# Optimization experiments

Hardware: AMD Instinct MI355X
Metric: run time of the kernel (lower is better)

The kernel has to match this reference:

```python
import jax, jax.numpy as jnp
import numpy as np


def setup_inputs() -> dict:
    key = jax.random.key(0)
    k1, k2, k3, k4 = jax.random.split(key, 4)
    N, F, E, M = 50000, 128, 1600000, 1024
    return {
        "molec_feature_vectures": jax.random.normal(k1, (N, F), dtype=jnp.float32),
        "W": jax.random.normal(k2, (F, F), dtype=jnp.float32),
        "mo_neighbour_indices": jax.random.randint(k3, (2, E), 0, N, dtype=jnp.int64),
        "mo_mol_id": jax.random.randint(k4, (E,), 0, M, dtype=jnp.int64),
        "n_output": M,
    }


def reference(molec_feature_vectures, W, mo_neighbour_indices, mo_mol_id, n_output):
    # Gather endpoint features for each neighbor pair: [E, F]
    fi = molec_feature_vectures[mo_neighbour_indices[0]]
    fj = molec_feature_vectures[mo_neighbour_indices[1]]
    # Symmetric bilinear form (mode='pes'): s_n = fi_n . (W + W^T) . fj_n
    Ws = W + W.T  # [F, F]
    # Fuse as (fi @ Ws) * fj summed over F to avoid a 3-operand einsum blowup
    scalars = jnp.einsum('ni,ij,nj->n', fi, Ws, fj)  # [E]
    # Segment-sum per molecule
    res = jax.ops.segment_sum(scalars, mo_mol_id, num_segments=n_output)  # [M]
    return res
```

## Files before the change

### kernel.cpp

```cpp
#include <hip/hip_runtime.h>
#include <hip/hip_bf16.h>

#define FDIM 128
#define BROWS 32
#define NBLK 256
#define NSLICE 32

typedef __attribute__((ext_vector_type(8))) short short8v;
typedef __attribute__((ext_vector_type(4))) float f32x4;
typedef __attribute__((ext_vector_type(2))) _Float16 half2v;

static __device__ __forceinline__ unsigned short f2bf(float x) {
    unsigned u = __float_as_uint(x);
    unsigned r = 0x7fffu + ((u >> 16) & 1u);
    return (unsigned short)((u + r) >> 16);
}
static __device__ __forceinline__ float bf2f(unsigned short h) {
    return __uint_as_float((unsigned)h << 16);
}
static __device__ __forceinline__ void split2(float v, short& h, short& l) {
    unsigned short hh = f2bf(v);
    h = (short)hh;
    l = (short)f2bf(v - bf2f(hh));
}

static __device__ __forceinline__ half2v u2h(unsigned u) {
    union { unsigned u; half2v h; } c; c.u = u; return c.h;
}
static __device__ __forceinline__ unsigned pack2h(float a, float b) {
    union { unsigned u; half2v h; } c;
    c.h[0] = (_Float16)a; c.h[1] = (_Float16)b; return c.u;
}
static __device__ __forceinline__ unsigned short f2h(float x) {
    union { unsigned short s; _Float16 h; } c; c.h = (_Float16)x; return c.s;
}
static __device__ __forceinline__ float fdot2(half2v a, half2v b, float c) {
#if defined(__has_builtin) && __has_builtin(__builtin_amdgcn_fdot2)
    return __builtin_amdgcn_fdot2(a, b, c, false);
#else
    return fmaf((float)a[1], (float)b[1], fmaf((float)a[0], (float)b[0], c));
#endif
}

__global__ __launch_bounds__(1024) void k_ws_hist(
    const float* __restrict__ W,
    unsigned short* __restrict__ WsH, unsigned short* __restrict__ WsL,
    const int* __restrict__ idx, int E, int nb, unsigned* __restrict__ M) {
    if (blockIdx.x >= NBLK) {
        int i2 = (blockIdx.x - NBLK) * 1024 + threadIdx.x;
        int i = i2 >> 7, j = i2 & 127;
        float w = W[i2] + W[j * 128 + i];
        short h, l;
        split2(w, h, l);
        WsH[i2] = (unsigned short)h;
        WsL[i2] = (unsigned short)l;
        return;
    }
    extern __shared__ unsigned cnt[];
    for (int i = threadIdx.x; i < nb; i += 1024) cnt[i] = 0;
    __syncthreads();
    int chunk = (E + NBLK - 1) / NBLK;
    int s = blockIdx.x * chunk;
    int e_end = min(E, s + chunk);
    for (int e = s + threadIdx.x; e < e_end; e += 1024) {
        int i1 = idx[E + e];
        atomicAdd(&cnt[i1 >> 5], 1u);
    }
    __syncthreads();
    for (int i = threadIdx.x; i < nb; i += 1024)
        M[(size_t)blockIdx.x * nb + i] = cnt[i];
}

__global__ __launch_bounds__(512, 4) void gemm_mfma(
    const float* __restrict__ Fm,
    const unsigned short* __restrict__ WsH, const unsigned short* __restrict__ WsL,
    unsigned short* __restrict__ Gh, int N) {
    __shared__ __align__(16) unsigned short sH[128 * 136];
    __shared__ __align__(16) unsigned short sL[128 * 136];

    for (int k = threadIdx.x; k < 128 * 16; k += 512) {
        int i = k >> 4, g = k & 15;
        *(uint4*)((char*)sH + i * 272 + g * 16) =
            *(const uint4*)((const char*)WsH + i * 256 + g * 16);
        *(uint4*)((char*)sL + i * 272 + g * 16) =
            *(const uint4*)((const char*)WsL + i * 256 + g * 16);
    }
    __syncthreads();

    const int wid  = threadIdx.x >> 6;
    const int lane = threadIdx.x & 63;
    const int ar   = lane & 15;
    const int kg   = lane >> 4;
    const int row0 = blockIdx.x * 128 + wid * 16;
    const int gr   = row0 + ar;
    const bool rv  = gr < N;
    const float* fp = Fm + (size_t)gr * FDIM;

    f32x4 acc[8];
#pragma unroll
    for (int t = 0; t < 8; ++t) acc[t] = (f32x4){0.f, 0.f, 0.f, 0.f};

#pragma unroll
    for (int ks = 0; ks < 4; ++ks) {
        const int k0 = ks * 32 + kg * 8;
        float4 fa = make_float4(0.f, 0.f, 0.f, 0.f);
        float4 fb = make_float4(0.f, 0.f, 0.f, 0.f);
        if (rv) {
            fa = *(const float4*)(fp + k0);
            fb = *(const float4*)(fp + k0 + 4);
        }
        short8v ah, al;
        {
            short h, l;
            split2(fa.x, h, l); ah[0] = h; al[0] = l;
            split2(fa.y, h, l); ah[1] = h; al[1] = l;
            split2(fa.z, h, l); ah[2] = h; al[2] = l;
            split2(fa.w, h, l); ah[3] = h; al[3] = l;
            split2(fb.x, h, l); ah[4] = h; al[4] = l;
            split2(fb.y, h, l); ah[5] = h; al[5] = l;
            split2(fb.z, h, l); ah[6] = h; al[6] = l;
            split2(fb.w, h, l); ah[7] = h; al[7] = l;
        }
#pragma unroll
        for (int ct = 0; ct < 8; ++ct) {
            const short8v bh = *(const short8v*)(sH + (ct * 16 + ar) * 136 + k0);
            const short8v bl = *(const short8v*)(sL + (ct * 16 + ar) * 136 + k0);
            acc[ct] = __builtin_amdgcn_mfma_f32_16x16x32_bf16(ah, bh, acc[ct], 0, 0, 0);
            acc[ct] = __builtin_amdgcn_mfma_f32_16x16x32_bf16(ah, bl, acc[ct], 0, 0, 0);
            acc[ct] = __builtin_amdgcn_mfma_f32_16x16x32_bf16(al, bh, acc[ct], 0, 0, 0);
        }
    }

#pragma unroll
    for (int r = 0; r < 4; ++r) {
        const int orow = row0 + kg * 4 + r;
        if (orow < N) {
#pragma unroll
            for (int ct = 0; ct < 8; ++ct)
                Gh[(size_t)orow * FDIM + ct * 16 + ar] = f2h(acc[ct][r]);
        }
    }
}

__global__ __launch_bounds__(256) void k_mscan2(unsigned* __restrict__ M, int nb,
                                                unsigned* __restrict__ tot) {
    int b = blockIdx.x * 4 + (threadIdx.x >> 6);
    int lane = threadIdx.x & 63;
    if (b >= nb) return;
    unsigned m0 = M[(size_t)(4 * lane + 0) * nb + b];
    unsigned m1 = M[(size_t)(4 * lane + 1) * nb + b];
    unsigned m2 = M[(size_t)(4 * lane + 2) * nb + b];
    unsigned m3 = M[(size_t)(4 * lane + 3) * nb + b];
    unsigned s = m0 + m1 + m2 + m3;
    unsigned incl = s;
#pragma unroll
    for (int d = 1; d < 64; d <<= 1) {
        unsigned u = __shfl_up(incl, d, 64);
        if (lane >= d) incl += u;
    }
    unsigned run = incl - s;
    M[(size_t)(4 * lane + 0) * nb + b] = run; run += m0;
    M[(size_t)(4 * lane + 1) * nb + b] = run; run += m1;
    M[(size_t)(4 * lane + 2) * nb + b] = run; run += m2;
    M[(size_t)(4 * lane + 3) * nb + b] = run;
    if (lane == 63) tot[b] = incl;
}

__global__ __launch_bounds__(1024) void k_scatter(const int* __restrict__ idx,
                                                  const int* __restrict__ mol, int E,
                                                  int nb, const unsigned* __restrict__ M,
                                                  const unsigned* __restrict__ tot,
                                                  unsigned* __restrict__ bucketStart,
                                                  unsigned* __restrict__ sortedE) {
    extern __shared__ unsigned cur[];
    __shared__ unsigned wTot[16];

    const int t = threadIdx.x;
    const int lane = t & 63, wid = t >> 6;
    const int b0 = 2 * t;
    unsigned a0 = (b0 < nb) ? tot[b0] : 0u;
    unsigned a1 = (b0 + 1 < nb) ? tot[b0 + 1] : 0u;
    unsigned tsum = a0 + a1;
    unsigned incl = tsum;
#pragma unroll
    for (int d = 1; d < 64; d <<= 1) {
        unsigned u = __shfl_up(incl, d, 64);
        if (lane >= d) incl += u;
    }
    if (lane == 63) wTot[wid] = incl;
    __syncthreads();
    unsigned wOff = 0;
    for (int i = 0; i < wid; ++i) wOff += wTot[i];
    const unsigned base = wOff + incl - tsum;
    if (b0 < nb)     cur[b0]     = M[(size_t)blockIdx.x * nb + b0] + base;
    if (b0 + 1 < nb) cur[b0 + 1] = M[(size_t)blockIdx.x * nb + b0 + 1] + base + a0;
    if (blockIdx.x == 0) {
        if (b0 < nb)     bucketStart[b0]     = base;
        if (b0 + 1 < nb) bucketStart[b0 + 1] = base + a0;
        if (t == 1023)   bucketStart[nb]     = wOff + incl;
    }
    __syncthreads();

    int chunk = (E + NBLK - 1) / NBLK;
    int s = blockIdx.x * chunk;
    int e_end = min(E, s + chunk);
    for (int e = s + threadIdx.x; e < e_end; e += 1024) {
        int i0 = idx[e];
        int i1 = idx[E + e];
        int m  = mol[e];
        int b  = i1 >> 5;
        int loc = i1 & 31;
        unsigned pos = atomicAdd(&cur[b], 1u);
        sortedE[pos] = (unsigned)i0 | ((unsigned)m << 16) | ((unsigned)loc << 26);
    }
}

__global__ __launch_bounds__(512, 6) void edge_kernel(
    const unsigned short* __restrict__ Gh, const float* __restrict__ Fm,
    const unsigned* __restrict__ sortedE, const unsigned* __restrict__ bucketStart,
    float* __restrict__ part, int N, int Mout) {
    __shared__ __align__(16) unsigned short sFrow[BROWS * FDIM];
    __shared__ float smol[1024];

    const int b = blockIdx.x;
    const int row0 = b * BROWS;
    const int nrow = min(BROWS, N - row0);

    for (int k = threadIdx.x; k < nrow * 16; k += 512) {
        int r = k >> 4, g = k & 15;
        const float4* src = (const float4*)(Fm + (size_t)(row0 + r) * FDIM + g * 8);
        float4 v0 = src[0], v1 = src[1];
        uint4 u;
        u.x = pack2h(v0.x, v0.y);
        u.y = pack2h(v0.z, v0.w);
        u.z = pack2h(v1.x, v1.y);
        u.w = pack2h(v1.z, v1.w);
        *(uint4*)(sFrow + r * FDIM + g * 8) = u;
    }
    for (int i = threadIdx.x; i < 1024; i += 512) smol[i] = 0.f;
    __syncthreads();

    const int s = (int)bucketStart[b];
    const int e_end = (int)bucketStart[b + 1];
    const int lane = threadIdx.x & 63;
    const int sub  = lane >> 4;
    const int t16  = lane & 15;
    const int off16 = t16 * 8;
    const int wid  = threadIdx.x >> 6;

#define DOT8(p, g, f) \
    p = fdot2(u2h((g).x), u2h((f).x), p); \
    p = fdot2(u2h((g).y), u2h((f).y), p); \
    p = fdot2(u2h((g).z), u2h((f).z), p); \
    p = fdot2(u2h((g).w), u2h((f).w), p);

    int base = s + wid * 16;

    unsigned pc0 = 0u, pc1 = 0u, pc2 = 0u, pc3 = 0u;
    unsigned pn0 = 0u, pn1 = 0u, pn2 = 0u, pn3 = 0u;
    if (base + sub < e_end)      pc0 = sortedE[base + sub];
    if (base + 4 + sub < e_end)  pc1 = sortedE[base + 4 + sub];
    if (base + 8 + sub < e_end)  pc2 = sortedE[base + 8 + sub];
    if (base + 12 + sub < e_end) pc3 = sortedE[base + 12 + sub];
    {
        const int nx = base + 128;
        if (nx + sub < e_end)      pn0 = sortedE[nx + sub];
        if (nx + 4 + sub < e_end)  pn1 = sortedE[nx + 4 + sub];
        if (nx + 8 + sub < e_end)  pn2 = sortedE[nx + 8 + sub];
        if (nx + 12 + sub < e_end) pn3 = sortedE[nx + 12 + sub];
    }
    uint4 gc0 = *(const uint4*)(Gh + (size_t)(pc0 & 0xffffu) * FDIM + off16);
    uint4 gc1 = *(const uint4*)(Gh + (size_t)(pc1 & 0xffffu) * FDIM + off16);
    uint4 gc2 = *(const uint4*)(Gh + (size_t)(pc2 & 0xffffu) * FDIM + off16);
    uint4 gc3 = *(const uint4*)(Gh + (size_t)(pc3 & 0xffffu) * FDIM + off16);

    while (base < e_end) {
        const uint4 gn0 = *(const uint4*)(Gh + (size_t)(pn0 & 0xffffu) * FDIM + off16);
        const uint4 gn1 = *(const uint4*)(Gh + (size_t)(pn1 & 0xffffu) * FDIM + off16);
        const uint4 gn2 = *(const uint4*)(Gh + (size_t)(pn2 & 0xffffu) * FDIM + off16);
        const uint4 gn3 = *(const uint4*)(Gh + (size_t)(pn3 & 0xffffu) * FDIM + off16);
        const int pf = base + 256;
        unsigned p20 = 0u, p21 = 0u, p22 = 0u, p23 = 0u;
        if (pf + sub < e_end)      p20 = sortedE[pf + sub];
        if (pf + 4 + sub < e_end)  p21 = sortedE[pf + 4 + sub];
        if (pf + 8 + sub < e_end)  p22 = sortedE[pf + 8 + sub];
        if (pf + 12 + sub < e_end) p23 = sortedE[pf + 12 + sub];

        const uint4 f0 = *(const uint4*)(sFrow + (pc0 >> 26) * FDIM + off16);
        const uint4 f1 = *(const uint4*)(sFrow + (pc1 >> 26) * FDIM + off16);
        const uint4 fv2 = *(const uint4*)(sFrow + (pc2 >> 26) * FDIM + off16);
        const uint4 f3 = *(const uint4*)(sFrow + (pc3 >> 26) * FDIM + off16);

        float p0 = 0.f, p1 = 0.f, p2 = 0.f, p3 = 0.f;
        DOT8(p0, gc0, f0);
        DOT8(p1, gc1, f1);
        DOT8(p2, gc2, fv2);
        DOT8(p3, gc3, f3);

        p0 += __shfl_xor(p0, 1, 16);
        p1 += __shfl_xor(p1, 1, 16);
        p2 += __shfl_xor(p2, 1, 16);
        p3 += __shfl_xor(p3, 1, 16);
        p0 += __shfl_xor(p0, 2, 16);
        p1 += __shfl_xor(p1, 2, 16);
        p2 += __shfl_xor(p2, 2, 16);
        p3 += __shfl_xor(p3, 2, 16);
        p0 += __shfl_xor(p0, 4, 16);
        p1 += __shfl_xor(p1, 4, 16);
        p2 += __shfl_xor(p2, 4, 16);
        p3 += __shfl_xor(p3, 4, 16);
        p0 += __shfl_xor(p0, 8, 16);
        p1 += __shfl_xor(p1, 8, 16);
        p2 += __shfl_xor(p2, 8, 16);
        p3 += __shfl_xor(p3, 8, 16);

        if (t16 == 0) {
            if (base + sub < e_end)      atomicAdd(&smol[(pc0 >> 16) & 0x3ff], p0);
            if (base + 4 + sub < e_end)  atomicAdd(&smol[(pc1 >> 16) & 0x3ff], p1);
            if (base + 8 + sub < e_end)  atomicAdd(&smol[(pc2 >> 16) & 0x3ff], p2);
            if (base + 12 + sub < e_end) atomicAdd(&smol[(pc3 >> 16) & 0x3ff], p3);
        }
        gc0 = gn0; gc1 = gn1; gc2 = gn2; gc3 = gn3;
        pc0 = pn0; pc1 = pn1; pc2 = pn2; pc3 = pn3;
        pn0 = p20; pn1 = p21; pn2 = p22; pn3 = p23;
        base += 128;
    }
#undef DOT8
    __syncthreads();

    float* prow = part + (size_t)b * 1024;
    for (int i = threadIdx.x; i < Mout; i += 512) prow[i] = smol[i];
}

__global__ __launch_bounds__(256) void k_red1(const float* __restrict__ part, int nb,
                                              float* __restrict__ partial, int Mout) {
    int gid = blockIdx.x * 256 + threadIdx.x;
    int m = gid & 1023;
    int sl = gid >> 10;
    int per = (nb + NSLICE - 1) / NSLICE;
    int b0 = sl * per;
    int b1 = min(nb, b0 + per);
    float s = 0.f;
    if (m < Mout) {
        for (int b = b0; b < b1; ++b) s += part[(size_t)b * 1024 + m];
    }
    partial[sl * 1024 + m] = s;
}

__global__ __launch_bounds__(256) void k_red2(const float* __restrict__ partial,
                                              float* __restrict__ out, int Mout) {
    int m = blockIdx.x * 256 + threadIdx.x;
    if (m < Mout) {
        float s = 0.f;
        for (int sl = 0; sl < NSLICE; ++sl) s += partial[sl * 1024 + m];
        out[m] = s;
    }
}

extern "C" void kernel_launch(void* const* d_in, const int* in_sizes, int n_in,
                              void* d_out, int out_size, void* d_ws, size_t ws_size,
                              hipStream_t stream) {
    const float* Fm = (const float*)d_in[0];
    const float* W  = (const float*)d_in[1];
    const int* idx  = (const int*)d_in[2];
    const int* mol  = (const int*)d_in[3];
    float* out = (float*)d_out;

    const int N = in_sizes[0] / FDIM;
    const int E = in_sizes[3];

    const int nb = (N + BROWS - 1) / BROWS;

    char* ws = (char*)d_ws;
    size_t o = 0;
    unsigned short* WsH = (unsigned short*)(ws + o); o += 32 * 1024;
    unsigned short* WsL = (unsigned short*)(ws + o); o += 32 * 1024;
    unsigned short* Gh = (unsigned short*)(ws + o);  o += ((size_t)N * FDIM * 2 + 255) & ~(size_t)255;
    unsigned* sortedE = (unsigned*)(ws + o);         o += ((size_t)E * 4 + 255) & ~(size_t)255;
    unsigned* M = (unsigned*)(ws + o);               o += ((size_t)NBLK * nb * 4 + 255) & ~(size_t)255;
    unsigned* tot = (unsigned*)(ws + o);             o += ((size_t)nb * 4 + 255) & ~(size_t)255;
    unsigned* bucketStart = (unsigned*)(ws + o);     o += ((size_t)(nb + 1) * 4 + 255) & ~(size_t)255;
    float* part = (float*)(ws + o);                  o += (size_t)nb * 1024 * sizeof(float);
    float* partial = (float*)(ws + o);               o += NSLICE * 1024 * sizeof(float);

    size_t smem = (size_t)nb * 4;
    k_ws_hist<<<NBLK + 16, 1024, smem, stream>>>(W, WsH, WsL, idx, E, nb, M);
    gemm_mfma<<<(N + 127) / 128, 512, 0, stream>>>(Fm, WsH, WsL, Gh, N);
    k_mscan2<<<(nb + 3) / 4, 256, 0, stream>>>(M, nb, tot);
    k_scatter<<<NBLK, 1024, smem, stream>>>(idx, mol, E, nb, M, tot, bucketStart, sortedE);

    edge_kernel<<<nb, 512, 0, stream>>>(Gh, Fm, sortedE, bucketStart, part, N, out_size);

    k_red1<<<NSLICE * 4, 256, 0, stream>>>(part, nb, partial, out_size);
    k_red2<<<(out_size + 255) / 256, 256, 0, stream>>>(partial, out, out_size);
}
```

Measured before the change: 195.8 us.

## Sub-bin edges by source row range within each destination bucket

The counting sort gains a secondary key: each 32-row destination bucket is split into 7 sub-bins by the high bits of the source index, so edges inside a bucket are ordered by source region. The goal is better cache locality when edge_kernel gathers source-side features. To keep the larger histogram (about 11k bins) within shared memory, the number of histogram blocks is halved, and a new single-block scan kernel computes bin and bucket starts. The costs are a bigger histogram and scan, an extra serial launch, and less parallelism in the histogram and scatter kernels.

New measurement: 244.5 us. 24.8% more time.

```diff
diff --git a/kernel.cpp b/kernel.cpp
--- a/kernel.cpp
+++ b/kernel.cpp
@@ -3,7 +3,8 @@
 
 #define FDIM 128
 #define BROWS 32
-#define NBLK 256
+#define NBLK 128
+#define NSUB 7
 #define NSLICE 32
 
 typedef __attribute__((ext_vector_type(8))) short short8v;
@@ -42,10 +43,14 @@
 #endif
 }
 
+static __device__ __forceinline__ int edge_bin(int i1, int i0) {
+    return (i1 >> 5) * NSUB + (i0 >> 13);
+}
+
 __global__ __launch_bounds__(1024) void k_ws_hist(
     const float* __restrict__ W,
     unsigned short* __restrict__ WsH, unsigned short* __restrict__ WsL,
-    const int* __restrict__ idx, int E, int nb, unsigned* __restrict__ M) {
+    const int* __restrict__ idx, int E, int nbins, unsigned* __restrict__ M) {
     if (blockIdx.x >= NBLK) {
         int i2 = (blockIdx.x - NBLK) * 1024 + threadIdx.x;
         int i = i2 >> 7, j = i2 & 127;
@@ -57,18 +62,19 @@
         return;
     }
     extern __shared__ unsigned cnt[];
-    for (int i = threadIdx.x; i < nb; i += 1024) cnt[i] = 0;
+    for (int i = threadIdx.x; i < nbins; i += 1024) cnt[i] = 0;
     __syncthreads();
     int chunk = (E + NBLK - 1) / NBLK;
     int s = blockIdx.x * chunk;
     int e_end = min(E, s + chunk);
     for (int e = s + threadIdx.x; e < e_end; e += 1024) {
         int i1 = idx[E + e];
-        atomicAdd(&cnt[i1 >> 5], 1u);
-    }
-    __syncthreads();
-    for (int i = threadIdx.x; i < nb; i += 1024)
-        M[(size_t)blockIdx.x * nb + i] = cnt[i];
+        int i0 = idx[e];
+        atomicAdd(&cnt[edge_bin(i1, i0)], 1u);
+    }
+    __syncthreads();
+    for (int i = threadIdx.x; i < nbins; i += 1024)
+        M[(size_t)blockIdx.x * nbins + i] = cnt[i];
 }
 
 __global__ __launch_bounds__(512, 4) void gemm_mfma(
@@ -142,16 +148,14 @@
     }
 }
 
-__global__ __launch_bounds__(256) void k_mscan2(unsigned* __restrict__ M, int nb,
+__global__ __launch_bounds__(256) void k_mscan2(unsigned* __restrict__ M, int nbins,
                                                 unsigned* __restrict__ tot) {
     int b = blockIdx.x * 4 + (threadIdx.x >> 6);
     int lane = threadIdx.x & 63;
-    if (b >= nb) return;
-    unsigned m0 = M[(size_t)(4 * lane + 0) * nb + b];
-    unsigned m1 = M[(size_t)(4 * lane + 1) * nb + b];
-    unsigned m2 = M[(size_t)(4 * lane + 2) * nb + b];
-    unsigned m3 = M[(size_t)(4 * lane + 3) * nb + b];
-    unsigned s = m0 + m1 + m2 + m3;
+    if (b >= nbins) return;
+    unsigned m0 = M[(size_t)(2 * lane + 0) * nbins + b];
+    unsigned m1 = M[(size_t)(2 * lane + 1) * nbins + b];
+    unsigned s = m0 + m1;
     unsigned incl = s;
 #pragma unroll
     for (int d = 1; d < 64; d <<= 1) {
@@ -159,48 +163,47 @@
         if (lane >= d) incl += u;
     }
     unsigned run = incl - s;
-    M[(size_t)(4 * lane + 0) * nb + b] = run; run += m0;
-    M[(size_t)(4 * lane + 1) * nb + b] = run; run += m1;
-    M[(size_t)(4 * lane + 2) * nb + b] = run; run += m2;
-    M[(size_t)(4 * lane + 3) * nb + b] = run;
+    M[(size_t)(2 * lane + 0) * nbins + b] = run; run += m0;
+    M[(size_t)(2 * lane + 1) * nbins + b] = run;
     if (lane == 63) tot[b] = incl;
 }
 
-__global__ __launch_bounds__(1024) void k_scatter(const int* __restrict__ idx,
-                                                  const int* __restrict__ mol, int E,
-                                                  int nb, const unsigned* __restrict__ M,
-                                                  const unsigned* __restrict__ tot,
-                                                  unsigned* __restrict__ bucketStart,
-                                                  unsigned* __restrict__ sortedE) {
-    extern __shared__ unsigned cur[];
-    __shared__ unsigned wTot[16];
-
+__global__ __launch_bounds__(256) void k_bscan_big(
+    const unsigned* __restrict__ tot, int nbins, int nb, int E,
+    unsigned* __restrict__ binStart, unsigned* __restrict__ bucketStart) {
+    __shared__ unsigned wS[4];
     const int t = threadIdx.x;
-    const int lane = t & 63, wid = t >> 6;
-    const int b0 = 2 * t;
-    unsigned a0 = (b0 < nb) ? tot[b0] : 0u;
-    unsigned a1 = (b0 + 1 < nb) ? tot[b0 + 1] : 0u;
-    unsigned tsum = a0 + a1;
-    unsigned incl = tsum;
-#pragma unroll
+    const int CE = (nbins + 255) >> 8;
+    const int a0 = t * CE;
+    const int a1 = min(nbins, a0 + CE);
+    unsigned s = 0;
+    for (int i = a0; i < a1; ++i) s += tot[i];
+    int lane = t & 63, wid = t >> 6;
+    unsigned incl = s;
     for (int d = 1; d < 64; d <<= 1) {
         unsigned u = __shfl_up(incl, d, 64);
         if (lane >= d) incl += u;
     }
-    if (lane == 63) wTot[wid] = incl;
+    if (lane == 63) wS[wid] = incl;
     __syncthreads();
     unsigned wOff = 0;
-    for (int i = 0; i < wid; ++i) wOff += wTot[i];
-    const unsigned base = wOff + incl - tsum;
-    if (b0 < nb)     cur[b0]     = M[(size_t)blockIdx.x * nb + b0] + base;
-    if (b0 + 1 < nb) cur[b0 + 1] = M[(size_t)blockIdx.x * nb + b0 + 1] + base + a0;
-    if (blockIdx.x == 0) {
-        if (b0 < nb)     bucketStart[b0]     = base;
-        if (b0 + 1 < nb) bucketStart[b0 + 1] = base + a0;
-        if (t == 1023)   bucketStart[nb]     = wOff + incl;
-    }
-    __syncthreads();
-
+    for (int i = 0; i < wid; ++i) wOff += wS[i];
+    unsigned run = wOff + incl - s;
+    for (int i = a0; i < a1; ++i) { binStart[i] = run; run += tot[i]; }
+    __syncthreads();
+    for (int b = t; b < nb; b += 256) bucketStart[b] = binStart[(size_t)b * NSUB];
+    if (t == 0) bucketStart[nb] = (unsigned)E;
+}
+
+__global__ __launch_bounds__(1024) void k_scatter(const int* __restrict__ idx,
+                                                  const int* __restrict__ mol, int E,
+                                                  int nbins, const unsigned* __restrict__ M,
+                                                  const unsigned* __restrict__ binStart,
+                                                  unsigned* __restrict__ sortedE) {
+    extern __shared__ unsigned cur[];
+    for (int i = threadIdx.x; i < nbins; i += 1024)
+        cur[i] = M[(size_t)blockIdx.x * nbins + i] + binStart[i];
+    __syncthreads();
     int chunk = (E + NBLK - 1) / NBLK;
     int s = blockIdx.x * chunk;
     int e_end = min(E, s + chunk);
@@ -208,9 +211,8 @@
         int i0 = idx[e];
         int i1 = idx[E + e];
         int m  = mol[e];
-        int b  = i1 >> 5;
         int loc = i1 & 31;
-        unsigned pos = atomicAdd(&cur[b], 1u);
+        unsigned pos = atomicAdd(&cur[edge_bin(i1, i0)], 1u);
         sortedE[pos] = (unsigned)i0 | ((unsigned)m << 16) | ((unsigned)loc << 26);
     }
 }
@@ -370,6 +372,7 @@
     const int E = in_sizes[3];
 
     const int nb = (N + BROWS - 1) / BROWS;
+    const int nbins = nb * NSUB;
 
     char* ws = (char*)d_ws;
     size_t o = 0;
@@ -377,17 +380,19 @@
     unsigned short* WsL = (unsigned short*)(ws + o); o += 32 * 1024;
     unsigned short* Gh = (unsigned short*)(ws + o);  o += ((size_t)N * FDIM * 2 + 255) & ~(size_t)255;
     unsigned* sortedE = (unsigned*)(ws + o);         o += ((size_t)E * 4 + 255) & ~(size_t)255;
-    unsigned* M = (unsigned*)(ws + o);               o += ((size_t)NBLK * nb * 4 + 255) & ~(size_t)255;
-    unsigned* tot = (unsigned*)(ws + o);             o += ((size_t)nb * 4 + 255) & ~(size_t)255;
+    unsigned* M = (unsigned*)(ws + o);               o += ((size_t)NBLK * nbins * 4 + 255) & ~(size_t)255;
+    unsigned* tot = (unsigned*)(ws + o);             o += ((size_t)nbins * 4 + 255) & ~(size_t)255;
+    unsigned* binStart = (unsigned*)(ws + o);        o += ((size_t)nbins * 4 + 255) & ~(size_t)255;
     unsigned* bucketStart = (unsigned*)(ws + o);     o += ((size_t)(nb + 1) * 4 + 255) & ~(size_t)255;
     float* part = (float*)(ws + o);                  o += (size_t)nb * 1024 * sizeof(float);
     float* partial = (float*)(ws + o);               o += NSLICE * 1024 * sizeof(float);
 
-    size_t smem = (size_t)nb * 4;
-    k_ws_hist<<<NBLK + 16, 1024, smem, stream>>>(W, WsH, WsL, idx, E, nb, M);
+    size_t smem = (size_t)nbins * 4;
+    k_ws_hist<<<NBLK + 16, 1024, smem, stream>>>(W, WsH, WsL, idx, E, nbins, M);
     gemm_mfma<<<(N + 127) / 128, 512, 0, stream>>>(Fm, WsH, WsL, Gh, N);
-    k_mscan2<<<(nb + 3) / 4, 256, 0, stream>>>(M, nb, tot);
-    k_scatter<<<NBLK, 1024, smem, stream>>>(idx, mol, E, nb, M, tot, bucketStart, sortedE);
+    k_mscan2<<<(nbins + 3) / 4, 256, 0, stream>>>(M, nbins, tot);
+    k_bscan_big<<<1, 256, 0, stream>>>(tot, nbins, nb, E, binStart, bucketStart);
+    k_scatter<<<NBLK, 1024, smem, stream>>>(idx, mol, E, nbins, M, binStart, sortedE);
 
     edge_kernel<<<nb, 512, 0, stream>>>(Gh, Fm, sortedE, bucketStart, part, N, out_size);
 
```
